# Performance work log

Measured on AMD Instinct MI355X. Metric: run time of the kernel, lower is better.

## Reference

```python
import jax, jax.numpy as jnp
import numpy as np

N_NODES = 100000
N_EDGES = 1200000
IN_FEATS = 64
OUT_FEATS = 64


def setup_inputs() -> dict:
    key = jax.random.key(0)
    k1, k2, k3, k4 = jax.random.split(key, 4)
    feature = jax.random.normal(k1, (N_NODES, IN_FEATS), dtype=jnp.float32)
    edge_src = jax.random.randint(k2, (N_EDGES,), 0, N_NODES, dtype=jnp.int32)
    edge_dst = jax.random.randint(k3, (N_EDGES,), 0, N_NODES, dtype=jnp.int32)
    # xavier_normal_ init for linear weight (fan_in=fan_out=64)
    std = float(np.sqrt(2.0 / (IN_FEATS + OUT_FEATS)))
    W = jax.random.normal(k4, (OUT_FEATS, IN_FEATS), dtype=jnp.float32) * std
    b = jnp.zeros((OUT_FEATS,), dtype=jnp.float32)
    return {"feature": feature, "edge_src": edge_src, "edge_dst": edge_dst, "W": W, "b": b}


def reference(feature, edge_src, edge_dst, W, b):
    # copy_src: gather source-node features per edge, then mean-reduce by dst.
    msgs = feature[edge_src]                                   # [E, d_in]
    summed = jax.ops.segment_sum(msgs, edge_dst, num_segments=N_NODES)  # [N, d_in]
    deg = jax.ops.segment_sum(jnp.ones((edge_src.shape[0],), feature.dtype),
                              edge_dst, num_segments=N_NODES)  # [N]
    h = summed / jnp.maximum(deg, 1.0)[:, None]                # mean; 0 for isolated nodes
    # apply_nodes: linear + activation
    h = jnp.einsum("nd,od->no", h, W) + b
    return jax.nn.relu(h)
```

## Files before the change

kernel.cpp:

```cpp
#include <hip/hip_runtime.h>


typedef __attribute__((ext_vector_type(8))) short short8;
typedef __attribute__((ext_vector_type(4))) float floatx4;

constexpr int kNodes = 100000;
constexpr int kEdges = 1200000;

constexpr int kBucketShift = 7;
constexpr int kBucketNodes = 1 << kBucketShift;
constexpr int kBuckets = (kNodes + kBucketNodes - 1) >> kBucketShift;

constexpr int kBinBlocks = 128;
constexpr int kEdgesPerBlock = kEdges / kBinBlocks;
constexpr int kEPT = (kEdgesPerBlock + 1023) / 1024;

constexpr int kCap = 3072;
constexpr float kFxScale = 262144.0f;
constexpr int kAccStride = 67;

constexpr int kWsOff    = 0;
constexpr int kWsBinned = kBinBlocks * 784;

__device__ __forceinline__ unsigned bf16rne(float f) {
  unsigned u = __float_as_uint(f);
  return (u + 0x7fffu + ((u >> 16) & 1u)) >> 16;
}

__global__ __launch_bounds__(1024) void gcn_build(
    const int* __restrict__ src, const int* __restrict__ dst,
    int* __restrict__ ws) {
  int* offT   = ws + kWsOff;
  int* binned = ws + kWsBinned;

  __shared__ int lhist[kBuckets];
  __shared__ int sm[1024];
  __shared__ int lcur[kBuckets];

  const int tid = threadIdx.x;
  for (int i = tid; i < kBuckets; i += 1024) lhist[i] = 0;
  __syncthreads();

  const int e0 = blockIdx.x * kEdgesPerBlock;
  int es[kEPT], ed[kEPT];
  #pragma unroll
  for (int k = 0; k < kEPT; ++k) {
    const int j = tid + k * 1024;
    if (j < kEdgesPerBlock) {
      es[k] = src[e0 + j];
      ed[k] = dst[e0 + j];
      atomicAdd(&lhist[ed[k] >> kBucketShift], 1);
    }
  }
  __syncthreads();

  const int own = (tid < kBuckets) ? lhist[tid] : 0;
  sm[tid] = own;
  __syncthreads();
  for (int off = 1; off < 1024; off <<= 1) {
    int v = (tid >= off) ? sm[tid - off] : 0;
    __syncthreads();
    sm[tid] += v;
    __syncthreads();
  }
  const int excl = sm[tid] - own;
  if (tid < kBuckets) {
    lcur[tid] = excl;
    offT[blockIdx.x * 784 + tid] = excl;
  }
  if (tid == kBuckets) offT[blockIdx.x * 784 + kBuckets] = kEdgesPerBlock;
  __syncthreads();

  int* myBin = binned + blockIdx.x * kEdgesPerBlock;
  #pragma unroll
  for (int k = 0; k < kEPT; ++k) {
    const int j = tid + k * 1024;
    if (j < kEdgesPerBlock) {
      const int d = ed[k];
      const int pos = atomicAdd(&lcur[d >> kBucketShift], 1);
      myBin[pos] = es[k] | ((d & (kBucketNodes - 1)) << 17);
    }
  }
}

__global__ __launch_bounds__(1024) void gcn_aggregate(
    const int*    __restrict__ ws_in,
    const float4* __restrict__ feat4,
    const float*  __restrict__ W,
    const float*  __restrict__ b,
    float*        __restrict__ out) {
  const int* offT   = ws_in + kWsOff;
  const int* binned = ws_in + kWsBinned;

  __shared__ __align__(16) char uShared[kBucketNodes * 72 * 2];
  __shared__ int    accum[kBucketNodes * kAccStride];
  __shared__ int    lofs[kBucketNodes + 1];
  __shared__ int    lcur[kBucketNodes];
  __shared__ int    runL[kBinBlocks + 1];
  __shared__ int    runG[kBinBlocks];
  __shared__ int    ssm[kBinBlocks];
  __shared__ ushort Wb16[64 * 64];
  __shared__ float  bsh[64];
  int*    lsrc  = (int*)uShared;
  ushort* hsAll = (ushort*)uShared;

  const int tid = threadIdx.x;
  const int bkt = blockIdx.x;

  if (tid < kBucketNodes) lcur[tid] = 0;
  for (int i = tid; i < 4096; i += 1024) Wb16[i] = (ushort)bf16rne(W[i]);
  if (tid < 64) bsh[tid] = b[tid];
  for (int i = tid; i < kBucketNodes * kAccStride; i += 1024) accum[i] = 0;

  int len = 0;
  if (tid < kBinBlocks) {
    const int o0 = offT[tid * 784 + bkt];
    const int o1 = offT[tid * 784 + bkt + 1];
    len = o1 - o0;
    runG[tid] = tid * kEdgesPerBlock + o0;
    ssm[tid] = len;
  }
  __syncthreads();
  for (int off = 1; off < kBinBlocks; off <<= 1) {
    int v = 0;
    if (tid < kBinBlocks && tid >= off) v = ssm[tid - off];
    __syncthreads();
    if (tid < kBinBlocks) ssm[tid] += v;
    __syncthreads();
  }
  if (tid < kBinBlocks) runL[tid] = ssm[tid] - len;
  if (tid == kBinBlocks - 1) runL[kBinBlocks] = ssm[kBinBlocks - 1];
  __syncthreads();

  int sz = runL[kBinBlocks];
  if (sz > kCap) sz = kCap;

  auto mapRead = [&](int j) -> unsigned {
    int lo = 0, hi = kBinBlocks;
    #pragma unroll
    for (int it = 0; it < 7; ++it) {
      const int mid = (lo + hi) >> 1;
      if (runL[mid] <= j) lo = mid; else hi = mid;
    }
    return (unsigned)binned[runG[lo] + (j - runL[lo])];
  };

  const int j0 = tid, j1 = tid + 1024, j2 = tid + 2048;
  const bool va = j0 < sz, vb = j1 < sz, vc = j2 < sz;
  unsigned ea = 0, eb = 0, ec = 0;
  if (va) { ea = mapRead(j0); atomicAdd(&lcur[ea >> 17], 1); }
  if (vb) { eb = mapRead(j1); atomicAdd(&lcur[eb >> 17], 1); }
  if (vc) { ec = mapRead(j2); atomicAdd(&lcur[ec >> 17], 1); }
  __syncthreads();

  if (tid < 64) {
    const int a  = lcur[tid * 2];
    const int b2 = lcur[tid * 2 + 1];
    int s = a + b2;
    #pragma unroll
    for (int off = 1; off < 64; off <<= 1) {
      const int v = __shfl_up(s, off, 64);
      if (tid >= off) s += v;
    }
    const int ex1 = s - b2;
    const int ex0 = ex1 - a;
    lofs[tid * 2]     = ex0;
    lofs[tid * 2 + 1] = ex1;
    lcur[tid * 2]     = ex0;
    lcur[tid * 2 + 1] = ex1;
    if (tid == 63) lofs[kBucketNodes] = s;
  }
  __syncthreads();

  if (va) { const int p = atomicAdd(&lcur[ea >> 17], 1); lsrc[p] = (int)ea; }
  if (vb) { const int p = atomicAdd(&lcur[eb >> 17], 1); lsrc[p] = (int)eb; }
  if (vc) { const int p = atomicAdd(&lcur[ec >> 17], 1); lsrc[p] = (int)ec; }
  __syncthreads();

  const int wave = tid >> 6;
  const int lane = tid & 63;
  const int g = lane >> 4;
  const int c = lane & 15;
  {
    const int E0 = lofs[wave * 8];
    const int E1 = lofs[wave * 8 + 8];
    const int lenw = E1 - E0;
    const int jb = E0 + ((lenw * g) >> 2);
    const int je = E0 + ((lenw * (g + 1)) >> 2);
    for (int j = jb; j < je; ++j) {
      const unsigned e = (unsigned)lsrc[j];
      const int s  = (int)(e & 0x1FFFF);
      const int dL = (int)(e >> 17);
      const float4 v = feat4[(size_t)s * 16 + c];
      int* row = accum + dL * kAccStride + 4 * c;
      atomicAdd(row + 0, (int)(v.x * kFxScale));
      atomicAdd(row + 1, (int)(v.y * kFxScale));
      atomicAdd(row + 2, (int)(v.z * kFxScale));
      atomicAdd(row + 3, (int)(v.w * kFxScale));
    }
  }
  __syncthreads();

  {
    const int nd = tid >> 3;
    const int ch = tid & 7;
    const int dg = lofs[nd + 1] - lofs[nd];
    const float inv = 1.0f / (kFxScale * (float)(dg > 1 ? dg : 1));
    const int* arow = accum + nd * kAccStride + ch * 8;
    unsigned h[8];
    #pragma unroll
    for (int q = 0; q < 8; ++q) h[q] = bf16rne((float)arow[q] * inv);
    uint4 pk;
    pk.x = h[0] | (h[1] << 16);
    pk.y = h[2] | (h[3] << 16);
    pk.z = h[4] | (h[5] << 16);
    pk.w = h[6] | (h[7] << 16);
    *(uint4*)(hsAll + nd * 72 + ch * 8) = pk;
  }
  __syncthreads();

  if (tid < 512) {
    const int w8   = tid >> 6;
    const int ln   = tid & 63;
    const int quad = ln >> 4;
    const int col  = ln & 15;
    const int n0 = bkt << kBucketShift;

    const short8 a0 = *reinterpret_cast<const short8*>(
        hsAll + (w8 * 16 + col) * 72 + 0 * 32 + quad * 8);
    const short8 a1 = *reinterpret_cast<const short8*>(
        hsAll + (w8 * 16 + col) * 72 + 1 * 32 + quad * 8);

    #pragma unroll
    for (int ob = 0; ob < 4; ++ob) {
      const short8 b0 = *reinterpret_cast<const short8*>(
          Wb16 + (ob * 16 + col) * 64 + 0 * 32 + quad * 8);
      const short8 b1 = *reinterpret_cast<const short8*>(
          Wb16 + (ob * 16 + col) * 64 + 1 * 32 + quad * 8);
      floatx4 acc = {0.f, 0.f, 0.f, 0.f};
      acc = __builtin_amdgcn_mfma_f32_16x16x32_bf16(a0, b0, acc, 0, 0, 0);
      acc = __builtin_amdgcn_mfma_f32_16x16x32_bf16(a1, b1, acc, 0, 0, 0);

      const int o = ob * 16 + col;
      const float bo = bsh[o];
      #pragma unroll
      for (int r = 0; r < 4; ++r) {
        const int node = n0 + w8 * 16 + quad * 4 + r;
        if (node < kNodes) {
          const float v = acc[r] + bo;
          out[(size_t)node * 64 + o] = v > 0.0f ? v : 0.0f;
        }
      }
    }
  }
}

extern "C" void kernel_launch(void* const* d_in, const int* in_sizes, int n_in,
                              void* d_out, int out_size, void* d_ws, size_t ws_size,
                              hipStream_t stream) {
  const float4* feat4    = (const float4*)d_in[0];
  const int*    edge_src = (const int*)   d_in[1];
  const int*    edge_dst = (const int*)   d_in[2];
  const float*  W        = (const float*) d_in[3];
  const float*  b        = (const float*) d_in[4];

  float* out = (float*)d_out;
  int*   ws  = (int*)d_ws;

  gcn_build<<<kBinBlocks, 1024, 0, stream>>>(edge_src, edge_dst, ws);
  gcn_aggregate<<<kBuckets, 1024, 0, stream>>>(ws, feat4, W, b, out);
}
```

Baseline: 146.3 us.

## Pre-convert node features to bf16 in build kernel to halve gather traffic

The build kernel now also converts the fp32 feature matrix to a packed bf16 copy in workspace, interleaving channels so each lane reads 8 bytes covering columns c, c+16, c+32, c+48. The aggregate kernel gathers from this bf16 copy instead of the fp32 features, halving bytes per random edge gather. The accumulator stride changes to 68 to match the new strided atomic pattern. It adds a full pass over the feature matrix (read 25.6MB, write 12.8MB) and lowers the precision of the summed inputs.

```diff
diff --git a/kernel.cpp b/kernel.cpp
--- a/kernel.cpp
+++ b/kernel.cpp
@@ -17,10 +17,11 @@
 
 constexpr int kCap = 3072;
 constexpr float kFxScale = 262144.0f;
-constexpr int kAccStride = 67;
-
-constexpr int kWsOff    = 0;
-constexpr int kWsBinned = kBinBlocks * 784;
+constexpr int kAccStride = 68;
+
+constexpr int kWsFeat   = 0;
+constexpr int kWsOff    = 3200000;
+constexpr int kWsBinned = kWsOff + kBinBlocks * 784;
 
 __device__ __forceinline__ unsigned bf16rne(float f) {
   unsigned u = __float_as_uint(f);
@@ -28,8 +29,10 @@
 }
 
 __global__ __launch_bounds__(1024) void gcn_build(
+    const float* __restrict__ feat,
     const int* __restrict__ src, const int* __restrict__ dst,
     int* __restrict__ ws) {
+  uint2* fb16  = (uint2*)(ws + kWsFeat);
   int* offT   = ws + kWsOff;
   int* binned = ws + kWsBinned;
 
@@ -52,6 +55,15 @@
       atomicAdd(&lhist[ed[k] >> kBucketShift], 1);
     }
   }
+
+  const int t = blockIdx.x * 1024 + tid;
+  for (int i = t; i < kNodes * 16; i += kBinBlocks * 1024) {
+    const float* fr = feat + (size_t)(i >> 4) * 64 + (i & 15);
+    uint2 p;
+    p.x = bf16rne(fr[0])  | (bf16rne(fr[16]) << 16);
+    p.y = bf16rne(fr[32]) | (bf16rne(fr[48]) << 16);
+    fb16[i] = p;
+  }
   __syncthreads();
 
   const int own = (tid < kBuckets) ? lhist[tid] : 0;
@@ -84,11 +96,11 @@
 }
 
 __global__ __launch_bounds__(1024) void gcn_aggregate(
-    const int*    __restrict__ ws_in,
-    const float4* __restrict__ feat4,
-    const float*  __restrict__ W,
-    const float*  __restrict__ b,
-    float*        __restrict__ out) {
+    const int*   __restrict__ ws_in,
+    const float* __restrict__ W,
+    const float* __restrict__ b,
+    float*       __restrict__ out) {
+  const uint2* fb16  = (const uint2*)(ws_in + kWsFeat);
   const int* offT   = ws_in + kWsOff;
   const int* binned = ws_in + kWsBinned;
 
@@ -191,12 +203,12 @@
       const unsigned e = (unsigned)lsrc[j];
       const int s  = (int)(e & 0x1FFFF);
       const int dL = (int)(e >> 17);
-      const float4 v = feat4[(size_t)s * 16 + c];
-      int* row = accum + dL * kAccStride + 4 * c;
-      atomicAdd(row + 0, (int)(v.x * kFxScale));
-      atomicAdd(row + 1, (int)(v.y * kFxScale));
-      atomicAdd(row + 2, (int)(v.z * kFxScale));
-      atomicAdd(row + 3, (int)(v.w * kFxScale));
+      const uint2 v = fb16[(size_t)s * 16 + c];
+      int* row = accum + dL * kAccStride + c;
+      atomicAdd(row + 0,  (int)(__uint_as_float(v.x << 16)          * kFxScale));
+      atomicAdd(row + 16, (int)(__uint_as_float(v.x & 0xffff0000u) * kFxScale));
+      atomicAdd(row + 32, (int)(__uint_as_float(v.y << 16)          * kFxScale));
+      atomicAdd(row + 48, (int)(__uint_as_float(v.y & 0xffff0000u) * kFxScale));
     }
   }
   __syncthreads();
@@ -258,15 +270,15 @@
 extern "C" void kernel_launch(void* const* d_in, const int* in_sizes, int n_in,
                               void* d_out, int out_size, void* d_ws, size_t ws_size,
                               hipStream_t stream) {
-  const float4* feat4    = (const float4*)d_in[0];
-  const int*    edge_src = (const int*)   d_in[1];
-  const int*    edge_dst = (const int*)   d_in[2];
-  const float*  W        = (const float*) d_in[3];
-  const float*  b        = (const float*) d_in[4];
+  const float* feature  = (const float*)d_in[0];
+  const int*   edge_src = (const int*)  d_in[1];
+  const int*   edge_dst = (const int*)  d_in[2];
+  const float* W        = (const float*)d_in[3];
+  const float* b        = (const float*)d_in[4];
 
   float* out = (float*)d_out;
   int*   ws  = (int*)d_ws;
 
-  gcn_build<<<kBinBlocks, 1024, 0, stream>>>(edge_src, edge_dst, ws);
-  gcn_aggregate<<<kBuckets, 1024, 0, stream>>>(ws, feat4, W, b, out);
-}
+  gcn_build<<<kBinBlocks, 1024, 0, stream>>>(feature, edge_src, edge_dst, ws);
+  gcn_aggregate<<<kBuckets, 1024, 0, stream>>>(ws, W, b, out);
+}
```

Result: faster. 138.2 us (-5.5%).
